# Performance work log

Measured on AMD Instinct MI355X. Metric: run time of the kernel, lower is better.

## Reference

```python
import jax, jax.numpy as jnp
import numpy as np

N = 50000
F_IN = 128
E = 800000
C = 32      # hidden_channels
H1 = 8      # heads_1
H2 = 1      # heads_2
NEG_SLOPE = 0.2


def setup_inputs() -> dict:
    key = jax.random.key(0)
    ks = jax.random.split(key, 16)
    s = 0.1
    x = jax.random.normal(ks[0], (N, F_IN), dtype=jnp.float32)
    edge_index = jax.random.randint(ks[1], (2, E), 0, N, dtype=jnp.int32)
    # layer 1: in=F_IN, out=C, heads=H1, concat=True
    Wl1 = jax.random.normal(ks[2], (H1 * C, F_IN), dtype=jnp.float32) * s
    bl1 = jnp.zeros((H1 * C,), dtype=jnp.float32)
    Wr1 = jax.random.normal(ks[3], (H1 * C, F_IN), dtype=jnp.float32) * s
    br1 = jnp.zeros((H1 * C,), dtype=jnp.float32)
    att1 = jax.random.normal(ks[4], (H1, C), dtype=jnp.float32) * s
    bias1 = jnp.zeros((H1 * C,), dtype=jnp.float32)
    # layer 2: in=H1*C, out=C, heads=H2, concat=False (mean)
    Wl2 = jax.random.normal(ks[5], (H2 * C, H1 * C), dtype=jnp.float32) * s
    bl2 = jnp.zeros((H2 * C,), dtype=jnp.float32)
    Wr2 = jax.random.normal(ks[6], (H2 * C, H1 * C), dtype=jnp.float32) * s
    br2 = jnp.zeros((H2 * C,), dtype=jnp.float32)
    att2 = jax.random.normal(ks[7], (H2, C), dtype=jnp.float32) * s
    bias2 = jnp.zeros((C,), dtype=jnp.float32)
    return {"x": x, "edge_index": edge_index,
            "Wl1": Wl1, "bl1": bl1, "Wr1": Wr1, "br1": br1, "att1": att1, "bias1": bias1,
            "Wl2": Wl2, "bl2": bl2, "Wr2": Wr2, "br2": br2, "att2": att2, "bias2": bias2}


def _gatv2_layer(x, src, dst, Wl, bl, Wr, br, att, bias, heads, out_c, concat):
    n = x.shape[0]
    xl = (x @ Wl.T + bl).reshape(n, heads, out_c)  # source transform
    xr = (x @ Wr.T + br).reshape(n, heads, out_c)  # target transform
    z = jax.nn.leaky_relu(xl[src] + xr[dst], NEG_SLOPE)          # [E, H, C]
    logit = jnp.einsum('ehc,hc->eh', z, att)                     # [E, H]
    # segment softmax over incoming edges of each target node
    m = jax.ops.segment_max(logit, dst, num_segments=n)          # [N, H]
    ex = jnp.exp(logit - m[dst])
    denom = jax.ops.segment_sum(ex, dst, num_segments=n)
    alpha = ex / jnp.maximum(denom[dst], 1e-16)                  # [E, H]
    out = jax.ops.segment_sum(alpha[..., None] * xl[src], dst, num_segments=n)  # [N, H, C]
    out = out.reshape(n, heads * out_c) if concat else out.mean(axis=1)
    return out + bias


def reference(x, edge_index, Wl1, bl1, Wr1, br1, att1, bias1,
              Wl2, bl2, Wr2, br2, att2, bias2):
    n = x.shape[0]
    # PyG GATv2Conv default: add self loops
    loops = jnp.arange(n, dtype=edge_index.dtype)
    src = jnp.concatenate([edge_index[0], loops])
    dst = jnp.concatenate([edge_index[1], loops])
    h = _gatv2_layer(x, src, dst, Wl1, bl1, Wr1, br1, att1, bias1, H1, C, True)
    h = jax.nn.gelu(h, approximate=False)
    out = _gatv2_layer(h, src, dst, Wl2, bl2, Wr2, br2, att2, bias2, H2, C, False)
    return out
```

## Files before the change

kernel.cpp:

```cpp
#include <hip/hip_runtime.h>
#include <hip/hip_bf16.h>


typedef unsigned short u16;
typedef short bf16x8 __attribute__((ext_vector_type(8)));
typedef float f32x4 __attribute__((ext_vector_type(4)));
typedef float f32x2 __attribute__((ext_vector_type(2)));

#define F_IN   128
#define CH     32
#define H1     8
#define JT1    512
#define JH1    256
#define JT2    64
#define JH2    32

#define OFF_Y1     0UL
#define OFF_XC     52000000UL
#define OFF_H      52000000UL
#define OFF_Y2     78000000UL
#define OFF_COL    85000000UL
#define OFF_DEG    89000000UL
#define OFF_ROW    89400000UL
#define OFF_CUR    89800000UL
#define OFF_WC     90200000UL
#define OFF_FLAG   90600000UL
#define OFF_BSUM   90700000UL
#define OFF_BOFF   90704096UL
#define WS_NEED    91000000UL

#define W_WL1   0
#define W_BL1   32768
#define W_WR1   33024
#define W_BR1   65792
#define W_ATT1  66048
#define W_BIAS1 66304
#define W_WL2   66560
#define W_BL2   74752
#define W_WR2   74784
#define W_BR2   82976
#define W_ATT2  83008
#define W_BIAS2 83040
#define W_TOTAL 83072

__device__ inline float b2f(u16 u) { return __uint_as_float(((unsigned)u) << 16); }
__device__ inline u16 f2b(float f) {
    unsigned u = __float_as_uint(f);
    unsigned r = (u + 0x7fffu + ((u >> 16) & 1u)) >> 16;
    return (u16)r;
}
__device__ inline unsigned cvtpk(float lo, float hi) {
    unsigned r;
    asm("v_cvt_pk_bf16_f32 %0, %1, %2" : "=v"(r) : "v"(lo), "v"(hi));
    return r;
}
__device__ inline f32x2 pk_add(f32x2 a, f32x2 b) {
    f32x2 d;
    asm("v_pk_add_f32 %0, %1, %2" : "=v"(d) : "v"(a), "v"(b));
    return d;
}
__device__ inline f32x2 pk_fma(f32x2 a, f32x2 b, f32x2 c) {
    f32x2 d;
    asm("v_pk_fma_f32 %0, %1, %2, %3" : "=v"(d) : "v"(a), "v"(b), "v"(c));
    return d;
}
__device__ inline f32x2 unpk(unsigned u) {
    f32x2 d;
    d.x = __uint_as_float(u << 16);
    d.y = __uint_as_float(u & 0xffff0000u);
    return d;
}
__device__ inline f32x2 pabs(f32x2 z) {
    f32x2 d;
    d.x = __uint_as_float(__float_as_uint(z.x) & 0x7fffffffu);
    d.y = __uint_as_float(__float_as_uint(z.y) & 0x7fffffffu);
    return d;
}

__global__ void detect_dtype(const u16* __restrict__ x, int* __restrict__ flag) {
    int lane = threadIdx.x;
    int cnt = 0;
    for (int i = lane; i < 512; i += 64) {
        u16 u = x[i];
        int e = (u >> 7) & 0xff;
        cnt += (u == 0 || (e >= 100 && e <= 141)) ? 1 : 0;
    }
#pragma unroll
    for (int m = 32; m; m >>= 1) cnt += __shfl_xor(cnt, m);
    if (lane == 0) *flag = (cnt >= 440) ? 1 : 0;
}

__global__ void cvt_bf16(const void* __restrict__ src, u16* __restrict__ dst,
                         int n, const int* __restrict__ flag) {
    int i = blockIdx.x * 256 + threadIdx.x;
    if (i >= n) return;
    if (*flag) dst[i] = ((const u16*)src)[i];
    else       dst[i] = f2b(((const float*)src)[i]);
}

struct WcArgs { const void* src[12]; int cum[13]; };

__global__ void cvt_weights(WcArgs a, u16* __restrict__ dst, int total,
                            const int* __restrict__ flag) {
    int i = blockIdx.x * 256 + threadIdx.x;
    if (i >= total) return;
    int s = 0;
    while (i >= a.cum[s + 1]) s++;
    int rel = i - a.cum[s];
    if (*flag) dst[i] = ((const u16*)a.src[s])[rel];
    else       dst[i] = f2b(((const float*)a.src[s])[rel]);
}

__global__ void build_deg(const int* __restrict__ ei, int* __restrict__ deg,
                          int E_, int NP) {
    int e = blockIdx.x * 256 + threadIdx.x;
    if (e >= E_ + NP) return;
    int dst = (e < E_) ? ei[E_ + e] : e - E_;
    atomicAdd(deg + dst, 1);
}

__global__ __launch_bounds__(256) void scan_part(const int* __restrict__ deg,
                                                 int* __restrict__ bsum, int NN) {
    __shared__ int red[256];
    int b = blockIdx.x, t = threadIdx.x;
    int base = b * 1024 + t * 4;
    int s = 0;
#pragma unroll
    for (int j = 0; j < 4; j++) { int i = base + j; if (i < NN) s += deg[i]; }
    red[t] = s; __syncthreads();
    for (int off = 128; off; off >>= 1) {
        if (t < off) red[t] += red[t + off];
        __syncthreads();
    }
    if (t == 0) bsum[b] = red[0];
}

__global__ __launch_bounds__(256) void scan_block(const int* __restrict__ bsum,
                                                  int* __restrict__ boff,
                                                  int* __restrict__ total_out, int NB) {
    __shared__ int ps[256];
    int t = threadIdx.x;
    int v = (t < NB) ? bsum[t] : 0;
    ps[t] = v; __syncthreads();
    for (int off = 1; off < 256; off <<= 1) {
        int x = (t >= off) ? ps[t - off] : 0;
        __syncthreads();
        ps[t] += x;
        __syncthreads();
    }
    if (t < NB) boff[t] = ps[t] - v;
    if (t == 255) *total_out = ps[255];
}

__global__ __launch_bounds__(256) void scan_final(const int* __restrict__ deg,
                                                  const int* __restrict__ boff,
                                                  int* __restrict__ rowptr,
                                                  int* __restrict__ cur, int NN) {
    __shared__ int ps[256];
    int b = blockIdx.x, t = threadIdx.x;
    int base = b * 1024 + t * 4;
    int v[4]; int s = 0;
#pragma unroll
    for (int j = 0; j < 4; j++) { int i = base + j; v[j] = (i < NN) ? deg[i] : 0; s += v[j]; }
    ps[t] = s; __syncthreads();
    for (int off = 1; off < 256; off <<= 1) {
        int x = (t >= off) ? ps[t - off] : 0;
        __syncthreads();
        ps[t] += x;
        __syncthreads();
    }
    int run = boff[b] + (t ? ps[t - 1] : 0);
#pragma unroll
    for (int j = 0; j < 4; j++) {
        int i = base + j;
        if (i < NN) { rowptr[i] = run; cur[i] = run; run += v[j]; }
    }
}

__global__ void scatter_edges(const int* __restrict__ ei, int* __restrict__ cur,
                              int* __restrict__ col, int E_, int NP) {
    int e = blockIdx.x * 256 + threadIdx.x;
    if (e >= E_ + NP) return;
    int src, dst;
    if (e < E_) { src = ei[e]; dst = ei[E_ + e]; }
    else        { src = dst = e - E_; }
    int pos = atomicAdd(cur + dst, 1);
    col[pos] = src;
}

template <int K>
__global__ __launch_bounds__(256) void gemm_mfma(
    const u16* __restrict__ X, const u16* __restrict__ Wl, const u16* __restrict__ Wr,
    const u16* __restrict__ bl, const u16* __restrict__ br,
    u16* __restrict__ Y, int M, int JH) {
    __shared__ float cs[4][32][68];
    const int t = threadIdx.x, w = t >> 6, l = t & 63;
    const int bm0 = blockIdx.x * 128, bn0 = blockIdx.y * 64;
    const int JT = 2 * JH;
    const int lr = l & 15, lk = (l >> 4) * 8;

    const u16* ax[2];
#pragma unroll
    for (int mt = 0; mt < 2; mt++) {
        int row = bm0 + w * 32 + mt * 16 + lr;
        if (row >= M) row = M - 1;
        ax[mt] = X + (size_t)row * K + lk;
    }
    const u16* bx[4];
    float bv[4];
#pragma unroll
    for (int nt = 0; nt < 4; nt++) {
        int j = bn0 + nt * 16 + lr;
        const u16* wp = (j < JH) ? (Wl + (size_t)j * K) : (Wr + (size_t)(j - JH) * K);
        bx[nt] = wp + lk;
        bv[nt] = b2f(j < JH ? bl[j] : br[j - JH]);
    }

    f32x4 acc[2][4];
#pragma unroll
    for (int mt = 0; mt < 2; mt++)
#pragma unroll
        for (int nt = 0; nt < 4; nt++) acc[mt][nt] = (f32x4){0.f, 0.f, 0.f, 0.f};

#pragma unroll
    for (int k0 = 0; k0 < K; k0 += 32) {
        bf16x8 a[2], b[4];
#pragma unroll
        for (int mt = 0; mt < 2; mt++) a[mt] = *(const bf16x8*)(ax[mt] + k0);
#pragma unroll
        for (int nt = 0; nt < 4; nt++) b[nt] = *(const bf16x8*)(bx[nt] + k0);
#pragma unroll
        for (int mt = 0; mt < 2; mt++)
#pragma unroll
            for (int nt = 0; nt < 4; nt++)
                acc[mt][nt] = __builtin_amdgcn_mfma_f32_16x16x32_bf16(
                    a[mt], b[nt], acc[mt][nt], 0, 0, 0);
    }

#pragma unroll
    for (int mt = 0; mt < 2; mt++)
#pragma unroll
        for (int nt = 0; nt < 4; nt++)
#pragma unroll
            for (int r = 0; r < 4; r++)
                cs[w][mt * 16 + (l >> 4) * 4 + r][nt * 16 + lr] = acc[mt][nt][r] + bv[nt];

#pragma unroll
    for (int p = 0; p < 4; p++) {
        int rl = p * 8 + (l >> 3);
        int grow = bm0 + w * 32 + rl;
        if (grow < M) {
            const float* rp = &cs[w][rl][(l & 7) * 8];
            float4 v0 = *(const float4*)rp;
            float4 v1 = *(const float4*)(rp + 4);
            uint4 o;
            o.x = cvtpk(v0.x, v0.y); o.y = cvtpk(v0.z, v0.w);
            o.z = cvtpk(v1.x, v1.y); o.w = cvtpk(v1.z, v1.w);
            *(uint4*)(Y + (size_t)grow * JT + bn0 + (l & 7) * 8) = o;
        }
    }
}

__global__ __launch_bounds__(256, 4) void agg1(
    const u16* __restrict__ Y1, const int* __restrict__ rowptr,
    const int* __restrict__ col, const u16* __restrict__ att,
    const u16* __restrict__ bias, u16* __restrict__ hout, int NN) {
    const int wid = blockIdx.x * 4 + (threadIdx.x >> 6);
    if (wid >= NN) return;
    const int lane = threadIdx.x & 63, half = lane >> 5, hl = lane & 31;
    const int n = wid;

    f32x2 xr2[4], a06[4], a04[4];
    {
        uint4 rx = *(const uint4*)(Y1 + (size_t)n * JT1 + JH1 + hl * 8);
        uint4 ra = *(const uint4*)(att + hl * 8);
        unsigned ux[4] = {rx.x, rx.y, rx.z, rx.w};
        unsigned ua[4] = {ra.x, ra.y, ra.z, ra.w};
#pragma unroll
        for (int p = 0; p < 4; p++) {
            xr2[p] = unpk(ux[p]);
            f32x2 a = unpk(ua[p]);
            a06[p].x = 0.6f * a.x; a06[p].y = 0.6f * a.y;
            a04[p].x = 0.4f * a.x; a04[p].y = 0.4f * a.y;
        }
    }
    f32x2 acc2[4] = {{0.f,0.f},{0.f,0.f},{0.f,0.f},{0.f,0.f}};
    float dsum = 0.f;

    auto edge = [&](uint4 raw) {
        unsigned uw[4] = {raw.x, raw.y, raw.z, raw.w};
        f32x2 xl2[4];
        f32x2 p2 = {0.f, 0.f};
#pragma unroll
        for (int p = 0; p < 4; p++) {
            xl2[p] = unpk(uw[p]);
            f32x2 z = pk_add(xl2[p], xr2[p]);
            p2 = pk_fma(z, a06[p], p2);
            p2 = pk_fma(pabs(z), a04[p], p2);
        }
        float pl = p2.x + p2.y;
        pl += __shfl_xor(pl, 1); pl += __shfl_xor(pl, 2);
        float e = __expf(pl);
        dsum += e;
        f32x2 e2; e2.x = e; e2.y = e;
#pragma unroll
        for (int p = 0; p < 4; p++) acc2[p] = pk_fma(e2, xl2[p], acc2[p]);
    };

    const int beg = rowptr[n], end = rowptr[n + 1];
    int i = beg + half;
    for (; i + 14 < end; i += 16) {
        int s[8];
#pragma unroll
        for (int k = 0; k < 8; k++) s[k] = col[i + 2 * k];
        uint4 r[8];
#pragma unroll
        for (int k = 0; k < 8; k++) r[k] = *(const uint4*)(Y1 + (size_t)s[k] * JT1 + hl * 8);
#pragma unroll
        for (int k = 0; k < 8; k++) edge(r[k]);
    }
    for (; i + 6 < end; i += 8) {
        int s0 = col[i], s1 = col[i + 2], s2 = col[i + 4], s3 = col[i + 6];
        uint4 r0 = *(const uint4*)(Y1 + (size_t)s0 * JT1 + hl * 8);
        uint4 r1 = *(const uint4*)(Y1 + (size_t)s1 * JT1 + hl * 8);
        uint4 r2 = *(const uint4*)(Y1 + (size_t)s2 * JT1 + hl * 8);
        uint4 r3 = *(const uint4*)(Y1 + (size_t)s3 * JT1 + hl * 8);
        edge(r0); edge(r1); edge(r2); edge(r3);
    }
    for (; i < end; i += 2) {
        uint4 r0 = *(const uint4*)(Y1 + (size_t)col[i] * JT1 + hl * 8);
        edge(r0);
    }

    dsum += __shfl_xor(dsum, 32);
#pragma unroll
    for (int p = 0; p < 4; p++) {
        acc2[p].x += __shfl_xor(acc2[p].x, 32);
        acc2[p].y += __shfl_xor(acc2[p].y, 32);
    }

    if (half == 0) {
        float inv = 1.f / fmaxf(dsum, 1e-16f);
        u16 bu[8];
        *(uint4*)bu = *(const uint4*)(bias + hl * 8);
        float v[8];
#pragma unroll
        for (int p = 0; p < 4; p++) {
            float x0 = acc2[p].x * inv + b2f(bu[2 * p]);
            float x1 = acc2[p].y * inv + b2f(bu[2 * p + 1]);
            v[2 * p]     = 0.5f * x0 * (1.f + erff(x0 * 0.70710678118654752f));
            v[2 * p + 1] = 0.5f * x1 * (1.f + erff(x1 * 0.70710678118654752f));
        }
        uint4 o;
        o.x = cvtpk(v[0], v[1]); o.y = cvtpk(v[2], v[3]);
        o.z = cvtpk(v[4], v[5]); o.w = cvtpk(v[6], v[7]);
        *(uint4*)(hout + (size_t)n * JH1 + hl * 8) = o;
    }
}

__global__ __launch_bounds__(256) void agg2(
    const u16* __restrict__ Y2, const int* __restrict__ rowptr,
    const int* __restrict__ col, const u16* __restrict__ att,
    const u16* __restrict__ bias, void* __restrict__ dout, int NN,
    const int* __restrict__ flag) {
    const int wid = blockIdx.x * 4 + (threadIdx.x >> 6);
    const int lane = threadIdx.x & 63;
    if (wid >= NN) return;
    const int n = wid, half = lane >> 5, c = lane & 31;

    float xr = b2f(Y2[(size_t)n * JT2 + JH2 + c]);
    float attv = b2f(att[c]);
    float acc = 0.f, dsum = 0.f;

    auto edge = [&](float xl) {
        float z = xl + xr;
        z = fmaf(0.4f, fabsf(z), 0.6f * z);
        float p = z * attv;
        p += __shfl_xor(p, 1); p += __shfl_xor(p, 2); p += __shfl_xor(p, 4);
        p += __shfl_xor(p, 8); p += __shfl_xor(p, 16);
        float e = __expf(p);
        dsum += e;
        acc += e * xl;
    };

    const int beg = rowptr[n], end = rowptr[n + 1];
    int i = beg + half;
    for (; i + 14 < end; i += 16) {
        int s[8];
#pragma unroll
        for (int k = 0; k < 8; k++) s[k] = col[i + 2 * k];
        float x[8];
#pragma unroll
        for (int k = 0; k < 8; k++) x[k] = b2f(Y2[(size_t)s[k] * JT2 + c]);
#pragma unroll
        for (int k = 0; k < 8; k++) edge(x[k]);
    }
    for (; i + 6 < end; i += 8) {
        int s0 = col[i], s1 = col[i + 2], s2 = col[i + 4], s3 = col[i + 6];
        float x0 = b2f(Y2[(size_t)s0 * JT2 + c]);
        float x1 = b2f(Y2[(size_t)s1 * JT2 + c]);
        float x2 = b2f(Y2[(size_t)s2 * JT2 + c]);
        float x3 = b2f(Y2[(size_t)s3 * JT2 + c]);
        edge(x0); edge(x1); edge(x2); edge(x3);
    }
    for (; i < end; i += 2) {
        edge(b2f(Y2[(size_t)col[i] * JT2 + c]));
    }

    acc += __shfl_xor(acc, 32);
    dsum += __shfl_xor(dsum, 32);
    if (half == 0) {
        float v = acc / fmaxf(dsum, 1e-16f) + b2f(bias[c]);
        int idx = n * JH2 + c;
        if (*flag) ((u16*)dout)[idx] = f2b(v);
        else       ((float*)dout)[idx] = v;
    }
}

extern "C" void kernel_launch(void* const* d_in, const int* in_sizes, int n_in,
                              void* d_out, int out_size, void* d_ws, size_t ws_size,
                              hipStream_t stream) {
    const int NN = in_sizes[0] / F_IN;
    const int EE = in_sizes[1] / 2;
    const int EP = EE + NN;
    if (ws_size < WS_NEED) return;

    char* w = (char*)d_ws;
    u16*   Y1   = (u16*)(w + OFF_Y1);
    u16*   XC   = (u16*)(w + OFF_XC);
    u16*   hbuf = (u16*)(w + OFF_H);
    u16*   Y2   = (u16*)(w + OFF_Y2);
    int*   col  = (int*)(w + OFF_COL);
    int*   deg  = (int*)(w + OFF_DEG);
    int*   rowp = (int*)(w + OFF_ROW);
    int*   cur  = (int*)(w + OFF_CUR);
    u16*   Wc   = (u16*)(w + OFF_WC);
    int*   flag = (int*)(w + OFF_FLAG);
    int*   bsum = (int*)(w + OFF_BSUM);
    int*   boff = (int*)(w + OFF_BOFF);

    const int* ei = (const int*)d_in[1];

    detect_dtype<<<1, 64, 0, stream>>>((const u16*)d_in[0], flag);
    cvt_bf16<<<(NN * F_IN + 255) / 256, 256, 0, stream>>>(d_in[0], XC, NN * F_IN, flag);
    {
        WcArgs a;
        int sizes[12] = {JH1 * F_IN, JH1, JH1 * F_IN, JH1, H1 * CH, JH1,
                         JH2 * JH1, JH2, JH2 * JH1, JH2, JH2, JH2};
        int c = 0;
        for (int s = 0; s < 12; s++) { a.src[s] = d_in[2 + s]; a.cum[s] = c; c += sizes[s]; }
        a.cum[12] = c;
        cvt_weights<<<(W_TOTAL + 255) / 256, 256, 0, stream>>>(a, Wc, W_TOTAL, flag);
    }

    const int NB = (NN + 1023) / 1024;
    hipMemsetAsync(deg, 0, (size_t)NN * 4, stream);
    build_deg<<<(EP + 255) / 256, 256, 0, stream>>>(ei, deg, EE, NN);
    scan_part<<<NB, 256, 0, stream>>>(deg, bsum, NN);
    scan_block<<<1, 256, 0, stream>>>(bsum, boff, rowp + NN, NB);
    scan_final<<<NB, 256, 0, stream>>>(deg, boff, rowp, cur, NN);
    scatter_edges<<<(EP + 255) / 256, 256, 0, stream>>>(ei, cur, col, EE, NN);

    {
        dim3 grid((NN + 127) / 128, JT1 / 64);
        gemm_mfma<F_IN><<<grid, 256, 0, stream>>>(XC, Wc + W_WL1, Wc + W_WR1,
                                                  Wc + W_BL1, Wc + W_BR1, Y1, NN, JH1);
    }
    agg1<<<(NN + 3) / 4, 256, 0, stream>>>(Y1, rowp, col, Wc + W_ATT1,
                                           Wc + W_BIAS1, hbuf, NN);

    {
        dim3 grid((NN + 127) / 128, JT2 / 64);
        gemm_mfma<JH1><<<grid, 256, 0, stream>>>(hbuf, Wc + W_WL2, Wc + W_WR2,
                                                 Wc + W_BL2, Wc + W_BR2, Y2, NN, JH2);
    }
    agg2<<<(NN + 3) / 4, 256, 0, stream>>>(Y2, rowp, col, Wc + W_ATT2,
                                           Wc + W_BIAS2, d_out, NN, flag);
}
```

Measured before the change: 289.1 us.

## Fuse input conversion into GEMM, merge scan kernels, remap aggregation lanes

Removes the separate dtype-detect and full-input bf16 conversion kernels: detection moves into the weight-conversion kernel and the first GEMM reads fp32 or bf16 input directly, converting in registers. It also preloads all A fragments, folds the block-offset scan into scan_final, and remaps agg1/agg2 so each wave processes four edges at once with 16 lanes per edge. This cuts kernel launches and a full read/write pass over the input. In exchange, every GEMM column block re-converts the fp32 input and holds more registers, and agg1 loses its occupancy launch bound.

```diff
diff --git a/kernel.cpp b/kernel.cpp
--- a/kernel.cpp
+++ b/kernel.cpp
@@ -16,7 +16,6 @@
 #define JH2    32
 
 #define OFF_Y1     0UL
-#define OFF_XC     52000000UL
 #define OFF_H      52000000UL
 #define OFF_Y2     78000000UL
 #define OFF_COL    85000000UL
@@ -26,7 +25,6 @@
 #define OFF_WC     90200000UL
 #define OFF_FLAG   90600000UL
 #define OFF_BSUM   90700000UL
-#define OFF_BOFF   90704096UL
 #define WS_NEED    91000000UL
 
 #define W_WL1   0
@@ -77,38 +75,38 @@
     return d;
 }
 
-__global__ void detect_dtype(const u16* __restrict__ x, int* __restrict__ flag) {
-    int lane = threadIdx.x;
-    int cnt = 0;
-    for (int i = lane; i < 512; i += 64) {
-        u16 u = x[i];
+struct WcArgs { const void* src[12]; int cum[13]; };
+
+__global__ __launch_bounds__(256) void cvt_weights(
+    WcArgs a, const u16* __restrict__ xprobe, u16* __restrict__ dst, int total,
+    int* __restrict__ flagOut) {
+    __shared__ int cnt[256];
+    __shared__ int sflag;
+    const int t = threadIdx.x;
+    int c = 0;
+    for (int i = t; i < 512; i += 256) {
+        u16 u = xprobe[i];
         int e = (u >> 7) & 0xff;
-        cnt += (u == 0 || (e >= 100 && e <= 141)) ? 1 : 0;
-    }
-#pragma unroll
-    for (int m = 32; m; m >>= 1) cnt += __shfl_xor(cnt, m);
-    if (lane == 0) *flag = (cnt >= 440) ? 1 : 0;
-}
-
-__global__ void cvt_bf16(const void* __restrict__ src, u16* __restrict__ dst,
-                         int n, const int* __restrict__ flag) {
-    int i = blockIdx.x * 256 + threadIdx.x;
-    if (i >= n) return;
-    if (*flag) dst[i] = ((const u16*)src)[i];
-    else       dst[i] = f2b(((const float*)src)[i]);
-}
-
-struct WcArgs { const void* src[12]; int cum[13]; };
-
-__global__ void cvt_weights(WcArgs a, u16* __restrict__ dst, int total,
-                            const int* __restrict__ flag) {
-    int i = blockIdx.x * 256 + threadIdx.x;
+        c += (u == 0 || (e >= 100 && e <= 141)) ? 1 : 0;
+    }
+    cnt[t] = c; __syncthreads();
+    for (int off = 128; off; off >>= 1) {
+        if (t < off) cnt[t] += cnt[t + off];
+        __syncthreads();
+    }
+    if (t == 0) {
+        sflag = (cnt[0] >= 440) ? 1 : 0;
+        if (blockIdx.x == 0) *flagOut = sflag;
+    }
+    __syncthreads();
+    const int fl = sflag;
+    int i = blockIdx.x * 256 + t;
     if (i >= total) return;
     int s = 0;
     while (i >= a.cum[s + 1]) s++;
     int rel = i - a.cum[s];
-    if (*flag) dst[i] = ((const u16*)a.src[s])[rel];
-    else       dst[i] = f2b(((const float*)a.src[s])[rel]);
+    if (fl) dst[i] = ((const u16*)a.src[s])[rel];
+    else    dst[i] = f2b(((const float*)a.src[s])[rel]);
 }
 
 __global__ void build_deg(const int* __restrict__ ei, int* __restrict__ deg,
@@ -135,29 +133,23 @@
     if (t == 0) bsum[b] = red[0];
 }
 
-__global__ __launch_bounds__(256) void scan_block(const int* __restrict__ bsum,
-                                                  int* __restrict__ boff,
-                                                  int* __restrict__ total_out, int NB) {
-    __shared__ int ps[256];
-    int t = threadIdx.x;
-    int v = (t < NB) ? bsum[t] : 0;
-    ps[t] = v; __syncthreads();
-    for (int off = 1; off < 256; off <<= 1) {
-        int x = (t >= off) ? ps[t - off] : 0;
-        __syncthreads();
-        ps[t] += x;
-        __syncthreads();
-    }
-    if (t < NB) boff[t] = ps[t] - v;
-    if (t == 255) *total_out = ps[255];
-}
-
-__global__ __launch_bounds__(256) void scan_final(const int* __restrict__ deg,
-                                                  const int* __restrict__ boff,
-                                                  int* __restrict__ rowptr,
-                                                  int* __restrict__ cur, int NN) {
+__global__ __launch_bounds__(256) void scan_final(
+    const int* __restrict__ deg, const int* __restrict__ bsum,
+    int* __restrict__ rowptr, int* __restrict__ cur, int NN, int NB) {
+    __shared__ int sb[256];
     __shared__ int ps[256];
     int b = blockIdx.x, t = threadIdx.x;
+    int bv = (t < NB) ? bsum[t] : 0;
+    sb[t] = bv; __syncthreads();
+    for (int off = 1; off < 256; off <<= 1) {
+        int x = (t >= off) ? sb[t - off] : 0;
+        __syncthreads();
+        sb[t] += x;
+        __syncthreads();
+    }
+    if (b == 0 && t == 0) rowptr[NN] = sb[NB - 1];
+    int boff = (b == 0) ? 0 : sb[b - 1];
+
     int base = b * 1024 + t * 4;
     int v[4]; int s = 0;
 #pragma unroll
@@ -169,7 +161,7 @@
         ps[t] += x;
         __syncthreads();
     }
-    int run = boff[b] + (t ? ps[t - 1] : 0);
+    int run = boff + (t ? ps[t - 1] : 0);
 #pragma unroll
     for (int j = 0; j < 4; j++) {
         int i = base + j;
@@ -188,24 +180,51 @@
     col[pos] = src;
 }
 
-template <int K>
+template <int K, bool DYN>
 __global__ __launch_bounds__(256) void gemm_mfma(
-    const u16* __restrict__ X, const u16* __restrict__ Wl, const u16* __restrict__ Wr,
+    const void* __restrict__ X, const u16* __restrict__ Wl, const u16* __restrict__ Wr,
     const u16* __restrict__ bl, const u16* __restrict__ br,
-    u16* __restrict__ Y, int M, int JH) {
+    u16* __restrict__ Y, int M, int JH, const int* __restrict__ flagp) {
     __shared__ float cs[4][32][68];
     const int t = threadIdx.x, w = t >> 6, l = t & 63;
     const int bm0 = blockIdx.x * 128, bn0 = blockIdx.y * 64;
     const int JT = 2 * JH;
     const int lr = l & 15, lk = (l >> 4) * 8;
-
-    const u16* ax[2];
+    const int fl = DYN ? *flagp : 1;
+
+    int rowm[2];
 #pragma unroll
     for (int mt = 0; mt < 2; mt++) {
         int row = bm0 + w * 32 + mt * 16 + lr;
         if (row >= M) row = M - 1;
-        ax[mt] = X + (size_t)row * K + lk;
-    }
+        rowm[mt] = row;
+    }
+
+    constexpr int KK = K / 32;
+    bf16x8 afr[2][KK];
+    if (fl) {
+        const u16* xb = (const u16*)X;
+#pragma unroll
+        for (int mt = 0; mt < 2; mt++)
+#pragma unroll
+            for (int kk = 0; kk < KK; kk++)
+                afr[mt][kk] = *(const bf16x8*)(xb + (size_t)rowm[mt] * K + lk + kk * 32);
+    } else {
+        const float* xf = (const float*)X;
+#pragma unroll
+        for (int mt = 0; mt < 2; mt++)
+#pragma unroll
+            for (int kk = 0; kk < KK; kk++) {
+                const float* p = xf + (size_t)rowm[mt] * K + lk + kk * 32;
+                float4 v0 = *(const float4*)p;
+                float4 v1 = *(const float4*)(p + 4);
+                uint4 o;
+                o.x = cvtpk(v0.x, v0.y); o.y = cvtpk(v0.z, v0.w);
+                o.z = cvtpk(v1.x, v1.y); o.w = cvtpk(v1.z, v1.w);
+                afr[mt][kk] = *(bf16x8*)&o;
+            }
+    }
+
     const u16* bx[4];
     float bv[4];
 #pragma unroll
@@ -223,18 +242,16 @@
         for (int nt = 0; nt < 4; nt++) acc[mt][nt] = (f32x4){0.f, 0.f, 0.f, 0.f};
 
 #pragma unroll
-    for (int k0 = 0; k0 < K; k0 += 32) {
-        bf16x8 a[2], b[4];
-#pragma unroll
-        for (int mt = 0; mt < 2; mt++) a[mt] = *(const bf16x8*)(ax[mt] + k0);
-#pragma unroll
-        for (int nt = 0; nt < 4; nt++) b[nt] = *(const bf16x8*)(bx[nt] + k0);
+    for (int kk = 0; kk < KK; kk++) {
+        bf16x8 b[4];
+#pragma unroll
+        for (int nt = 0; nt < 4; nt++) b[nt] = *(const bf16x8*)(bx[nt] + kk * 32);
 #pragma unroll
         for (int mt = 0; mt < 2; mt++)
 #pragma unroll
             for (int nt = 0; nt < 4; nt++)
                 acc[mt][nt] = __builtin_amdgcn_mfma_f32_16x16x32_bf16(
-                    a[mt], b[nt], acc[mt][nt], 0, 0, 0);
+                    afr[mt][kk], b[nt], acc[mt][nt], 0, 0, 0);
     }
 
 #pragma unroll
@@ -261,100 +278,126 @@
     }
 }
 
-__global__ __launch_bounds__(256, 4) void agg1(
+__global__ __launch_bounds__(256) void agg1(
     const u16* __restrict__ Y1, const int* __restrict__ rowptr,
     const int* __restrict__ col, const u16* __restrict__ att,
     const u16* __restrict__ bias, u16* __restrict__ hout, int NN) {
     const int wid = blockIdx.x * 4 + (threadIdx.x >> 6);
     if (wid >= NN) return;
-    const int lane = threadIdx.x & 63, half = lane >> 5, hl = lane & 31;
+    const int lane = threadIdx.x & 63, le = lane >> 4, cl = lane & 15;
     const int n = wid;
 
-    f32x2 xr2[4], a06[4], a04[4];
-    {
-        uint4 rx = *(const uint4*)(Y1 + (size_t)n * JT1 + JH1 + hl * 8);
-        uint4 ra = *(const uint4*)(att + hl * 8);
+    f32x2 xr2[2][4], a06[2][4], a04[2][4];
+#pragma unroll
+    for (int h = 0; h < 2; h++) {
+        uint4 rx = *(const uint4*)(Y1 + (size_t)n * JT1 + JH1 + h * 128 + cl * 8);
+        uint4 ra = *(const uint4*)(att + h * 128 + cl * 8);
         unsigned ux[4] = {rx.x, rx.y, rx.z, rx.w};
         unsigned ua[4] = {ra.x, ra.y, ra.z, ra.w};
 #pragma unroll
         for (int p = 0; p < 4; p++) {
-            xr2[p] = unpk(ux[p]);
+            xr2[h][p] = unpk(ux[p]);
             f32x2 a = unpk(ua[p]);
-            a06[p].x = 0.6f * a.x; a06[p].y = 0.6f * a.y;
-            a04[p].x = 0.4f * a.x; a04[p].y = 0.4f * a.y;
-        }
-    }
-    f32x2 acc2[4] = {{0.f,0.f},{0.f,0.f},{0.f,0.f},{0.f,0.f}};
-    float dsum = 0.f;
-
-    auto edge = [&](uint4 raw) {
-        unsigned uw[4] = {raw.x, raw.y, raw.z, raw.w};
-        f32x2 xl2[4];
-        f32x2 p2 = {0.f, 0.f};
+            a06[h][p].x = 0.6f * a.x; a06[h][p].y = 0.6f * a.y;
+            a04[h][p].x = 0.4f * a.x; a04[h][p].y = 0.4f * a.y;
+        }
+    }
+    f32x2 acc2[2][4] = {{{0.f,0.f},{0.f,0.f},{0.f,0.f},{0.f,0.f}},
+                        {{0.f,0.f},{0.f,0.f},{0.f,0.f},{0.f,0.f}}};
+    float dsumA = 0.f, dsumB = 0.f;
+
+    auto edge = [&](uint4 r0, uint4 r1, bool act) {
+        unsigned u0[4] = {r0.x, r0.y, r0.z, r0.w};
+        unsigned u1[4] = {r1.x, r1.y, r1.z, r1.w};
+        f32x2 xl2[2][4];
+        f32x2 pa = {0.f, 0.f}, pb = {0.f, 0.f};
 #pragma unroll
         for (int p = 0; p < 4; p++) {
-            xl2[p] = unpk(uw[p]);
-            f32x2 z = pk_add(xl2[p], xr2[p]);
-            p2 = pk_fma(z, a06[p], p2);
-            p2 = pk_fma(pabs(z), a04[p], p2);
-        }
-        float pl = p2.x + p2.y;
-        pl += __shfl_xor(pl, 1); pl += __shfl_xor(pl, 2);
-        float e = __expf(pl);
-        dsum += e;
-        f32x2 e2; e2.x = e; e2.y = e;
-#pragma unroll
-        for (int p = 0; p < 4; p++) acc2[p] = pk_fma(e2, xl2[p], acc2[p]);
+            xl2[0][p] = unpk(u0[p]);
+            f32x2 z = pk_add(xl2[0][p], xr2[0][p]);
+            pa = pk_fma(z, a06[0][p], pa);
+            pa = pk_fma(pabs(z), a04[0][p], pa);
+        }
+#pragma unroll
+        for (int p = 0; p < 4; p++) {
+            xl2[1][p] = unpk(u1[p]);
+            f32x2 z = pk_add(xl2[1][p], xr2[1][p]);
+            pb = pk_fma(z, a06[1][p], pb);
+            pb = pk_fma(pabs(z), a04[1][p], pb);
+        }
+        float la = pa.x + pa.y;
+        la += __shfl_xor(la, 1); la += __shfl_xor(la, 2);
+        float lb = pb.x + pb.y;
+        lb += __shfl_xor(lb, 1); lb += __shfl_xor(lb, 2);
+        float ea = __expf(la), eb = __expf(lb);
+        if (!act) { ea = 0.f; eb = 0.f; }
+        dsumA += ea; dsumB += eb;
+        f32x2 ea2; ea2.x = ea; ea2.y = ea;
+        f32x2 eb2; eb2.x = eb; eb2.y = eb;
+#pragma unroll
+        for (int p = 0; p < 4; p++) {
+            acc2[0][p] = pk_fma(ea2, xl2[0][p], acc2[0][p]);
+            acc2[1][p] = pk_fma(eb2, xl2[1][p], acc2[1][p]);
+        }
     };
 
     const int beg = rowptr[n], end = rowptr[n + 1];
-    int i = beg + half;
-    for (; i + 14 < end; i += 16) {
-        int s[8];
-#pragma unroll
-        for (int k = 0; k < 8; k++) s[k] = col[i + 2 * k];
-        uint4 r[8];
-#pragma unroll
-        for (int k = 0; k < 8; k++) r[k] = *(const uint4*)(Y1 + (size_t)s[k] * JT1 + hl * 8);
-#pragma unroll
-        for (int k = 0; k < 8; k++) edge(r[k]);
-    }
-    for (; i + 6 < end; i += 8) {
-        int s0 = col[i], s1 = col[i + 2], s2 = col[i + 4], s3 = col[i + 6];
-        uint4 r0 = *(const uint4*)(Y1 + (size_t)s0 * JT1 + hl * 8);
-        uint4 r1 = *(const uint4*)(Y1 + (size_t)s1 * JT1 + hl * 8);
-        uint4 r2 = *(const uint4*)(Y1 + (size_t)s2 * JT1 + hl * 8);
-        uint4 r3 = *(const uint4*)(Y1 + (size_t)s3 * JT1 + hl * 8);
-        edge(r0); edge(r1); edge(r2); edge(r3);
-    }
-    for (; i < end; i += 2) {
-        uint4 r0 = *(const uint4*)(Y1 + (size_t)col[i] * JT1 + hl * 8);
-        edge(r0);
-    }
-
-    dsum += __shfl_xor(dsum, 32);
-#pragma unroll
-    for (int p = 0; p < 4; p++) {
-        acc2[p].x += __shfl_xor(acc2[p].x, 32);
-        acc2[p].y += __shfl_xor(acc2[p].y, 32);
-    }
-
-    if (half == 0) {
-        float inv = 1.f / fmaxf(dsum, 1e-16f);
-        u16 bu[8];
-        *(uint4*)bu = *(const uint4*)(bias + hl * 8);
-        float v[8];
+    int i = beg;
+    for (; i + 8 <= end; i += 8) {
+        int sA = col[i + le];
+        int sB = col[i + 4 + le];
+        const u16* pA = Y1 + (size_t)sA * JT1 + cl * 8;
+        const u16* pB = Y1 + (size_t)sB * JT1 + cl * 8;
+        uint4 rA0 = *(const uint4*)pA;
+        uint4 rA1 = *(const uint4*)(pA + 128);
+        uint4 rB0 = *(const uint4*)pB;
+        uint4 rB1 = *(const uint4*)(pB + 128);
+        edge(rA0, rA1, true);
+        edge(rB0, rB1, true);
+    }
+    for (; i < end; i += 4) {
+        int idx = i + le;
+        bool act = idx < end;
+        int s0 = col[act ? idx : end - 1];
+        const u16* p0 = Y1 + (size_t)s0 * JT1 + cl * 8;
+        uint4 r0 = *(const uint4*)p0;
+        uint4 r1 = *(const uint4*)(p0 + 128);
+        edge(r0, r1, act);
+    }
+
+    dsumA += __shfl_xor(dsumA, 16); dsumA += __shfl_xor(dsumA, 32);
+    dsumB += __shfl_xor(dsumB, 16); dsumB += __shfl_xor(dsumB, 32);
+#pragma unroll
+    for (int h = 0; h < 2; h++)
 #pragma unroll
         for (int p = 0; p < 4; p++) {
-            float x0 = acc2[p].x * inv + b2f(bu[2 * p]);
-            float x1 = acc2[p].y * inv + b2f(bu[2 * p + 1]);
-            v[2 * p]     = 0.5f * x0 * (1.f + erff(x0 * 0.70710678118654752f));
-            v[2 * p + 1] = 0.5f * x1 * (1.f + erff(x1 * 0.70710678118654752f));
-        }
-        uint4 o;
-        o.x = cvtpk(v[0], v[1]); o.y = cvtpk(v[2], v[3]);
-        o.z = cvtpk(v[4], v[5]); o.w = cvtpk(v[6], v[7]);
-        *(uint4*)(hout + (size_t)n * JH1 + hl * 8) = o;
+            acc2[h][p].x += __shfl_xor(acc2[h][p].x, 16);
+            acc2[h][p].x += __shfl_xor(acc2[h][p].x, 32);
+            acc2[h][p].y += __shfl_xor(acc2[h][p].y, 16);
+            acc2[h][p].y += __shfl_xor(acc2[h][p].y, 32);
+        }
+
+    if (le == 0) {
+        float invA = 1.f / fmaxf(dsumA, 1e-16f);
+        float invB = 1.f / fmaxf(dsumB, 1e-16f);
+#pragma unroll
+        for (int h = 0; h < 2; h++) {
+            float inv = h ? invB : invA;
+            u16 bu[8];
+            *(uint4*)bu = *(const uint4*)(bias + h * 128 + cl * 8);
+            float v[8];
+#pragma unroll
+            for (int p = 0; p < 4; p++) {
+                float x0 = acc2[h][p].x * inv + b2f(bu[2 * p]);
+                float x1 = acc2[h][p].y * inv + b2f(bu[2 * p + 1]);
+                v[2 * p]     = 0.5f * x0 * (1.f + erff(x0 * 0.70710678118654752f));
+                v[2 * p + 1] = 0.5f * x1 * (1.f + erff(x1 * 0.70710678118654752f));
+            }
+            uint4 o;
+            o.x = cvtpk(v[0], v[1]); o.y = cvtpk(v[2], v[3]);
+            o.z = cvtpk(v[4], v[5]); o.w = cvtpk(v[6], v[7]);
+            *(uint4*)(hout + (size_t)n * JH1 + h * 128 + cl * 8) = o;
+        }
     }
 }
 
@@ -364,56 +407,65 @@
     const u16* __restrict__ bias, void* __restrict__ dout, int NN,
     const int* __restrict__ flag) {
     const int wid = blockIdx.x * 4 + (threadIdx.x >> 6);
-    const int lane = threadIdx.x & 63;
     if (wid >= NN) return;
-    const int n = wid, half = lane >> 5, c = lane & 31;
-
-    float xr = b2f(Y2[(size_t)n * JT2 + JH2 + c]);
-    float attv = b2f(att[c]);
-    float acc = 0.f, dsum = 0.f;
-
-    auto edge = [&](float xl) {
-        float z = xl + xr;
-        z = fmaf(0.4f, fabsf(z), 0.6f * z);
-        float p = z * attv;
-        p += __shfl_xor(p, 1); p += __shfl_xor(p, 2); p += __shfl_xor(p, 4);
-        p += __shfl_xor(p, 8); p += __shfl_xor(p, 16);
-        float e = __expf(p);
+    const int lane = threadIdx.x & 63, le = lane >> 4, cl = lane & 15;
+    const int n = wid;
+
+    f32x2 xr2 = unpk(*(const unsigned*)(Y2 + (size_t)n * JT2 + JH2 + cl * 2));
+    f32x2 av  = unpk(*(const unsigned*)(att + cl * 2));
+    f32x2 a06; a06.x = 0.6f * av.x; a06.y = 0.6f * av.y;
+    f32x2 a04; a04.x = 0.4f * av.x; a04.y = 0.4f * av.y;
+    f32x2 acc2 = {0.f, 0.f};
+    float dsum = 0.f;
+
+    auto edge = [&](unsigned raw, bool act) {
+        f32x2 xl2 = unpk(raw);
+        f32x2 z = pk_add(xl2, xr2);
+        f32x2 p2 = pk_fma(z, a06, (f32x2){0.f, 0.f});
+        p2 = pk_fma(pabs(z), a04, p2);
+        float pl = p2.x + p2.y;
+        pl += __shfl_xor(pl, 1); pl += __shfl_xor(pl, 2);
+        pl += __shfl_xor(pl, 4); pl += __shfl_xor(pl, 8);
+        float e = __expf(pl);
+        if (!act) e = 0.f;
         dsum += e;
-        acc += e * xl;
+        f32x2 e2; e2.x = e; e2.y = e;
+        acc2 = pk_fma(e2, xl2, acc2);
     };
 
     const int beg = rowptr[n], end = rowptr[n + 1];
-    int i = beg + half;
-    for (; i + 14 < end; i += 16) {
-        int s[8];
-#pragma unroll
-        for (int k = 0; k < 8; k++) s[k] = col[i + 2 * k];
-        float x[8];
-#pragma unroll
-        for (int k = 0; k < 8; k++) x[k] = b2f(Y2[(size_t)s[k] * JT2 + c]);
-#pragma unroll
-        for (int k = 0; k < 8; k++) edge(x[k]);
-    }
-    for (; i + 6 < end; i += 8) {
-        int s0 = col[i], s1 = col[i + 2], s2 = col[i + 4], s3 = col[i + 6];
-        float x0 = b2f(Y2[(size_t)s0 * JT2 + c]);
-        float x1 = b2f(Y2[(size_t)s1 * JT2 + c]);
-        float x2 = b2f(Y2[(size_t)s2 * JT2 + c]);
-        float x3 = b2f(Y2[(size_t)s3 * JT2 + c]);
-        edge(x0); edge(x1); edge(x2); edge(x3);
-    }
-    for (; i < end; i += 2) {
-        edge(b2f(Y2[(size_t)col[i] * JT2 + c]));
-    }
-
-    acc += __shfl_xor(acc, 32);
-    dsum += __shfl_xor(dsum, 32);
-    if (half == 0) {
-        float v = acc / fmaxf(dsum, 1e-16f) + b2f(bias[c]);
-        int idx = n * JH2 + c;
-        if (*flag) ((u16*)dout)[idx] = f2b(v);
-        else       ((float*)dout)[idx] = v;
+    int i = beg;
+    for (; i + 8 <= end; i += 8) {
+        int sA = col[i + le];
+        int sB = col[i + 4 + le];
+        unsigned rA = *(const unsigned*)(Y2 + (size_t)sA * JT2 + cl * 2);
+        unsigned rB = *(const unsigned*)(Y2 + (size_t)sB * JT2 + cl * 2);
+        edge(rA, true);
+        edge(rB, true);
+    }
+    for (; i < end; i += 4) {
+        int idx = i + le;
+        bool act = idx < end;
+        int s0 = col[act ? idx : end - 1];
+        unsigned r0 = *(const unsigned*)(Y2 + (size_t)s0 * JT2 + cl * 2);
+        edge(r0, act);
+    }
+
+    dsum += __shfl_xor(dsum, 16); dsum += __shfl_xor(dsum, 32);
+    acc2.x += __shfl_xor(acc2.x, 16); acc2.x += __shfl_xor(acc2.x, 32);
+    acc2.y += __shfl_xor(acc2.y, 16); acc2.y += __shfl_xor(acc2.y, 32);
+
+    if (le == 0) {
+        float inv = 1.f / fmaxf(dsum, 1e-16f);
+        f32x2 bv = unpk(*(const unsigned*)(bias + cl * 2));
+        float v0 = acc2.x * inv + bv.x;
+        float v1 = acc2.y * inv + bv.y;
+        if (*flag) {
+            *(unsigned*)((u16*)dout + n * JH2 + cl * 2) = cvtpk(v0, v1);
+        } else {
+            float2 o; o.x = v0; o.y = v1;
+            *(float2*)((float*)dout + n * JH2 + cl * 2) = o;
+        }
     }
 }
 
@@ -427,7 +479,6 @@
 
     char* w = (char*)d_ws;
     u16*   Y1   = (u16*)(w + OFF_Y1);
-    u16*   XC   = (u16*)(w + OFF_XC);
     u16*   hbuf = (u16*)(w + OFF_H);
     u16*   Y2   = (u16*)(w + OFF_Y2);
     int*   col  = (int*)(w + OFF_COL);
@@ -437,12 +488,9 @@
     u16*   Wc   = (u16*)(w + OFF_WC);
     int*   flag = (int*)(w + OFF_FLAG);
     int*   bsum = (int*)(w + OFF_BSUM);
-    int*   boff = (int*)(w + OFF_BOFF);
 
     const int* ei = (const int*)d_in[1];
 
-    detect_dtype<<<1, 64, 0, stream>>>((const u16*)d_in[0], flag);
-    cvt_bf16<<<(NN * F_IN + 255) / 256, 256, 0, stream>>>(d_in[0], XC, NN * F_IN, flag);
     {
         WcArgs a;
         int sizes[12] = {JH1 * F_IN, JH1, JH1 * F_IN, JH1, H1 * CH, JH1,
@@ -450,29 +498,29 @@
         int c = 0;
         for (int s = 0; s < 12; s++) { a.src[s] = d_in[2 + s]; a.cum[s] = c; c += sizes[s]; }
         a.cum[12] = c;
-        cvt_weights<<<(W_TOTAL + 255) / 256, 256, 0, stream>>>(a, Wc, W_TOTAL, flag);
+        cvt_weights<<<(W_TOTAL + 255) / 256, 256, 0, stream>>>(
+            a, (const u16*)d_in[0], Wc, W_TOTAL, flag);
     }
 
     const int NB = (NN + 1023) / 1024;
     hipMemsetAsync(deg, 0, (size_t)NN * 4, stream);
     build_deg<<<(EP + 255) / 256, 256, 0, stream>>>(ei, deg, EE, NN);
     scan_part<<<NB, 256, 0, stream>>>(deg, bsum, NN);
-    scan_block<<<1, 256, 0, stream>>>(bsum, boff, rowp + NN, NB);
-    scan_final<<<NB, 256, 0, stream>>>(deg, boff, rowp, cur, NN);
+    scan_final<<<NB, 256, 0, stream>>>(deg, bsum, rowp, cur, NN, NB);
     scatter_edges<<<(EP + 255) / 256, 256, 0, stream>>>(ei, cur, col, EE, NN);
 
     {
         dim3 grid((NN + 127) / 128, JT1 / 64);
-        gemm_mfma<F_IN><<<grid, 256, 0, stream>>>(XC, Wc + W_WL1, Wc + W_WR1,
-                                                  Wc + W_BL1, Wc + W_BR1, Y1, NN, JH1);
+        gemm_mfma<F_IN, true><<<grid, 256, 0, stream>>>(
+            d_in[0], Wc + W_WL1, Wc + W_WR1, Wc + W_BL1, Wc + W_BR1, Y1, NN, JH1, flag);
     }
     agg1<<<(NN + 3) / 4, 256, 0, stream>>>(Y1, rowp, col, Wc + W_ATT1,
                                            Wc + W_BIAS1, hbuf, NN);
 
     {
         dim3 grid((NN + 127) / 128, JT2 / 64);
-        gemm_mfma<JH1><<<grid, 256, 0, stream>>>(hbuf, Wc + W_WL2, Wc + W_WR2,
-                                                 Wc + W_BL2, Wc + W_BR2, Y2, NN, JH2);
+        gemm_mfma<JH1, false><<<grid, 256, 0, stream>>>(
+            hbuf, Wc + W_WL2, Wc + W_WR2, Wc + W_BL2, Wc + W_BR2, Y2, NN, JH2, flag);
     }
     agg2<<<(NN + 3) / 4, 256, 0, stream>>>(Y2, rowp, col, Wc + W_ATT2,
                                            Wc + W_BIAS2, d_out, NN, flag);
```

New measurement: 298.2 us. 1.03x slower.
